# Performance work log

Hardware: AMD Instinct MI355X
Metric: run time of the kernel (lower is better)

Reference implementation:

```python
import jax, jax.numpy as jnp
import numpy as np

EMBED_DIM = 1024
NUM_HEADS = 16
HEAD_DIM = EMBED_DIM // NUM_HEADS


def setup_inputs() -> dict:
    key = jax.random.key(0)
    ks = jax.random.split(key, 11)
    L, N, E = 2048, 4, EMBED_DIM
    s = 1.0 / np.sqrt(E)
    return {
        "query": jax.random.normal(ks[0], (L, N, E), jnp.float32),
        "key": jax.random.normal(ks[1], (L, N, E), jnp.float32),
        "value": jax.random.normal(ks[2], (L, N, E), jnp.float32),
        "Wq": jax.random.normal(ks[3], (E, E), jnp.float32) * s,
        "bq": jax.random.normal(ks[4], (E,), jnp.float32) * s,
        "Wk": jax.random.normal(ks[5], (E, E), jnp.float32) * s,
        "bk": jax.random.normal(ks[6], (E,), jnp.float32) * s,
        "Wv": jax.random.normal(ks[7], (E, E), jnp.float32) * s,
        "bv": jax.random.normal(ks[8], (E,), jnp.float32) * s,
        "Wo": jax.random.normal(ks[9], (E, E), jnp.float32) * s,
        "bo": jax.random.normal(ks[10], (E,), jnp.float32) * s,
    }


def reference(query, key, value, Wq, bq, Wk, bk, Wv, bv, Wo, bo):
    # query/key/value: [L, N, E] (seq-first, as in nn.MultiheadAttention)
    L, N, E = query.shape
    H, D = NUM_HEADS, HEAD_DIM
    scaling = float(D) ** -0.5

    # nn.Linear: x @ W.T + b
    q = (query @ Wq.T + bq) * scaling           # [L, N, E]
    k = key @ Wk.T + bk                          # [S, N, E]
    v = value @ Wv.T + bv                        # [S, N, E]

    S = k.shape[0]
    # [L, N, E] -> [N*H, L, D]
    q = q.reshape(L, N * H, D).transpose(1, 0, 2)
    k = k.reshape(S, N * H, D).transpose(1, 0, 2)
    v = v.reshape(S, N * H, D).transpose(1, 0, 2)

    # attention scores: [N*H, L, S]
    scores = jnp.einsum('bld,bsd->bls', q, k)
    attn = jax.nn.softmax(scores, axis=-1)       # dropout p=0.0 (eval)

    out = jnp.einsum('bls,bsd->bld', attn, v)    # [N*H, L, D]
    out = out.transpose(1, 0, 2).reshape(L, N, E)
    attn_output = out @ Wo.T + bo                # [L, N, E]

    # need_weights=True: average attention over heads -> [N, L, S]
    avg_weights = attn.reshape(N, H, L, S).sum(axis=1) / H
    return attn_output, avg_weights
```

## Files before the change

### kernel.cpp

```cpp
#include <hip/hip_runtime.h>
#include <stdint.h>


typedef __attribute__((ext_vector_type(8))) short bf16x8;
typedef __attribute__((ext_vector_type(4))) short s16x4;
typedef __attribute__((ext_vector_type(4))) float f32x4;

#define MFMA(a, b, c) __builtin_amdgcn_mfma_f32_16x16x32_bf16((a), (b), (c), 0, 0, 0)

__device__ __forceinline__ ushort f2bf(float f) {
    uint32_t u = __builtin_bit_cast(uint32_t, f);
    u += 0x7fffu + ((u >> 16) & 1u);
    return (ushort)(u >> 16);
}

__global__ __launch_bounds__(256) void k_prep(
    const float* __restrict__ xq, const float* __restrict__ xk, const float* __restrict__ xv,
    const float* __restrict__ wq, const float* __restrict__ wk,
    const float* __restrict__ wv, const float* __restrict__ wo,
    ushort* __restrict__ xqb, ushort* __restrict__ xkb, ushort* __restrict__ xvb,
    ushort* __restrict__ wqb, ushort* __restrict__ wkb,
    ushort* __restrict__ wvb, ushort* __restrict__ wob)
{
    const int z = blockIdx.y;
    const float* src; ushort* dst; int n8;
    switch (z) {
        case 0: src = xq; dst = xqb; n8 = 1048576; break;
        case 1: src = xk; dst = xkb; n8 = 1048576; break;
        case 2: src = xv; dst = xvb; n8 = 1048576; break;
        case 3: src = wq; dst = wqb; n8 = 131072;  break;
        case 4: src = wk; dst = wkb; n8 = 131072;  break;
        case 5: src = wv; dst = wvb; n8 = 131072;  break;
        default: src = wo; dst = wob; n8 = 131072; break;
    }
    int u = blockIdx.x * 256 + threadIdx.x;
    if (u >= n8) return;
    const float4* s4 = (const float4*)src;
    float4 a = s4[2 * (size_t)u];
    float4 b = s4[2 * (size_t)u + 1];
    uint4 o;
    o.x = (uint)f2bf(a.x) | ((uint)f2bf(a.y) << 16);
    o.y = (uint)f2bf(a.z) | ((uint)f2bf(a.w) << 16);
    o.z = (uint)f2bf(b.x) | ((uint)f2bf(b.y) << 16);
    o.w = (uint)f2bf(b.z) | ((uint)f2bf(b.w) << 16);
    *(uint4*)(dst + 8 * (size_t)u) = o;
}

__global__ __launch_bounds__(256) void k_proj(
    const ushort* __restrict__ Xq, const ushort* __restrict__ Xk, const ushort* __restrict__ Xv,
    const ushort* __restrict__ Wqb, const ushort* __restrict__ Wkb, const ushort* __restrict__ Wvb,
    const float* __restrict__ bq, const float* __restrict__ bk, const float* __restrict__ bv,
    ushort* __restrict__ Qa, ushort* __restrict__ Ka, ushort* __restrict__ Vt)
{
    const int z = blockIdx.z;
    const ushort* X = (z == 0) ? Xq : (z == 1) ? Xk : Xv;
    const ushort* W = (z == 0) ? Wqb : (z == 1) ? Wkb : Wvb;
    const float* B = (z == 0) ? bq : (z == 1) ? bk : bv;

    __shared__ __align__(16) ushort xt[128][40];
    __shared__ __align__(16) ushort wt[128][40];

    const int t = threadIdx.x;
    const int lane = t & 63;
    const int w = t >> 6;
    const int wr = w >> 1, wc = w & 1;
    const int c = lane & 15, g = lane >> 4;

    const int xrow0 = blockIdx.x * 128;
    const int wrow0 = blockIdx.y * 128;

    f32x4 acc[4][4] = {};

    for (int kt = 0; kt < 32; ++kt) {
        const int k0 = kt * 32;
        __syncthreads();
#pragma unroll
        for (int i = 0; i < 2; ++i) {
            int slot = t + i * 256;
            int row = slot >> 2, seg = slot & 3;
            *(uint4*)&xt[row][seg * 8] =
                *(const uint4*)(X + (size_t)(xrow0 + row) * 1024 + k0 + seg * 8);
            *(uint4*)&wt[row][seg * 8] =
                *(const uint4*)(W + (size_t)(wrow0 + row) * 1024 + k0 + seg * 8);
        }
        __syncthreads();

        const ushort (*At)[40] = (z == 2) ? wt : xt;
        const ushort (*Bt)[40] = (z == 2) ? xt : wt;
        bf16x8 af[4], bfr[4];
#pragma unroll
        for (int m = 0; m < 4; ++m) af[m]  = *(const bf16x8*)&At[wr * 64 + m * 16 + c][g * 8];
#pragma unroll
        for (int n = 0; n < 4; ++n) bfr[n] = *(const bf16x8*)&Bt[wc * 64 + n * 16 + c][g * 8];
#pragma unroll
        for (int m = 0; m < 4; ++m)
#pragma unroll
            for (int n = 0; n < 4; ++n)
                acc[m][n] = MFMA(af[m], bfr[n], acc[m][n]);
    }

    const float QS = 0.125f * 1.44269504088896340736f;
#pragma unroll
    for (int m = 0; m < 4; ++m)
#pragma unroll
        for (int n = 0; n < 4; ++n)
#pragma unroll
            for (int i = 0; i < 4; ++i) {
                int rowi = ((z == 2) ? wrow0 : xrow0) + wr * 64 + m * 16 + 4 * g + i;
                int coli = ((z == 2) ? xrow0 : wrow0) + wc * 64 + n * 16 + c;
                int e = (z == 2) ? rowi : coli;
                int r = (z == 2) ? coli : rowi;
                float v = acc[m][n][i] + B[e];
                if (z == 0) v *= QS;
                ushort bv16 = f2bf(v);
                int nn = r & 3, l = r >> 2, h = e >> 6, d = e & 63;
                int bh = nn * 16 + h;
                if (z == 2) Vt[((size_t)bh * 64 + d) * 2048 + l] = bv16;
                else {
                    ushort* o = (z == 0) ? Qa : Ka;
                    o[((size_t)bh * 2048 + l) * 64 + d] = bv16;
                }
            }
}

__global__ __launch_bounds__(512) void k_attn(
    const ushort* __restrict__ Qa, const ushort* __restrict__ Ka, const ushort* __restrict__ Vt,
    ushort* __restrict__ ctx, float* __restrict__ mbuf, float* __restrict__ lbuf)
{
    __shared__ __align__(16) ushort smem[4608 * 2 + 8 * 16 * 72];
    ushort (*kt)[72] = (ushort(*)[72])smem;
    ushort (*vt)[72] = (ushort(*)[72])(smem + 4608);

    const int t = threadIdx.x;
    const int lane = t & 63;
    const int w = t >> 6;
    const int c = lane & 15, g = lane >> 4;
    ushort* ptw = smem + 9216 + w * 1152;
    const int bh = blockIdx.y;
    const int n = bh >> 4, h = bh & 15;
    const int l0 = blockIdx.x * 128;
    const int lrow = l0 + w * 16 + c;

    bf16x8 aq0 = *(const bf16x8*)(Qa + ((size_t)bh * 2048 + lrow) * 64 + g * 8);
    bf16x8 aq1 = *(const bf16x8*)(Qa + ((size_t)bh * 2048 + lrow) * 64 + 32 + g * 8);

    f32x4 O[4] = {};
    float m = -1e30f, l = 0.f;

    for (int st = 0; st < 32; ++st) {
        __syncthreads();
        {
            int row = t >> 3, seg = t & 7;
            *(uint4*)&kt[row][seg * 8] =
                *(const uint4*)(Ka + ((size_t)bh * 2048 + st * 64 + row) * 64 + seg * 8);
            *(uint4*)&vt[row][seg * 8] =
                *(const uint4*)(Vt + ((size_t)bh * 64 + row) * 2048 + st * 64 + seg * 8);
        }
        __syncthreads();

        f32x4 sc[4];
#pragma unroll
        for (int ct = 0; ct < 4; ++ct) {
            bf16x8 kb0 = *(const bf16x8*)&kt[ct * 16 + c][g * 8];
            bf16x8 kb1 = *(const bf16x8*)&kt[ct * 16 + c][32 + g * 8];
            f32x4 z = {};
            z = MFMA(kb0, aq0, z);
            sc[ct] = MFMA(kb1, aq1, z);
        }

        float pm = fmaxf(fmaxf(sc[0][0], sc[0][1]), fmaxf(sc[0][2], sc[0][3]));
#pragma unroll
        for (int ct = 1; ct < 4; ++ct)
            pm = fmaxf(pm, fmaxf(fmaxf(sc[ct][0], sc[ct][1]), fmaxf(sc[ct][2], sc[ct][3])));
        pm = fmaxf(pm, __shfl_xor(pm, 16));
        pm = fmaxf(pm, __shfl_xor(pm, 32));

        float mn = fmaxf(m, pm);
        float al = exp2f(m - mn);
        m = mn;
        l *= al;
        O[0] *= al; O[1] *= al; O[2] *= al; O[3] *= al;

#pragma unroll
        for (int ct = 0; ct < 4; ++ct) {
            float p0 = exp2f(sc[ct][0] - m);
            float p1 = exp2f(sc[ct][1] - m);
            float p2 = exp2f(sc[ct][2] - m);
            float p3 = exp2f(sc[ct][3] - m);
            l += (p0 + p1) + (p2 + p3);
            uint pa, pb;
            asm("v_cvt_pk_bf16_f32 %0, %1, %2" : "=v"(pa) : "v"(p0), "v"(p1));
            asm("v_cvt_pk_bf16_f32 %0, %1, %2" : "=v"(pb) : "v"(p2), "v"(p3));
            uint64_t pk = (uint64_t)pa | ((uint64_t)pb << 32);
            *(s16x4*)&ptw[c * 72 + ct * 16 + g * 4] = __builtin_bit_cast(s16x4, pk);
        }

        bf16x8 ap0 = *(const bf16x8*)&ptw[c * 72 + g * 8];
        bf16x8 ap1 = *(const bf16x8*)&ptw[c * 72 + 32 + g * 8];
#pragma unroll
        for (int dt = 0; dt < 4; ++dt) {
            bf16x8 vb0 = *(const bf16x8*)&vt[dt * 16 + c][g * 8];
            bf16x8 vb1 = *(const bf16x8*)&vt[dt * 16 + c][32 + g * 8];
            O[dt] = MFMA(vb0, ap0, O[dt]);
            O[dt] = MFMA(vb1, ap1, O[dt]);
        }
    }

    float lsum = l;
    lsum += __shfl_xor(lsum, 16);
    lsum += __shfl_xor(lsum, 32);
    float rl = 1.0f / lsum;

    __syncthreads();
    float* otw = (float*)smem + w * 1040;
#pragma unroll
    for (int dt = 0; dt < 4; ++dt)
#pragma unroll
        for (int r = 0; r < 4; ++r)
            otw[c * 65 + dt * 16 + 4 * g + r] = O[dt][r] * rl;
#pragma unroll
    for (int qq = 0; qq < 16; ++qq) {
        float v = otw[qq * 65 + lane];
        int lr2 = l0 + w * 16 + qq;
        ctx[((size_t)lr2 * 4 + n) * 1024 + h * 64 + lane] = f2bf(v);
    }
    if (g == 0) {
        mbuf[(size_t)bh * 2048 + l0 + w * 16 + c] = m;
        lbuf[(size_t)bh * 2048 + l0 + w * 16 + c] = lsum;
    }
}

__global__ __launch_bounds__(256) void k_oproj(
    const ushort* __restrict__ ctx, const ushort* __restrict__ Wob,
    const float* __restrict__ bo, float* __restrict__ out)
{
    __shared__ __align__(16) ushort xt[128][40];
    __shared__ __align__(16) ushort wt[128][40];

    const int t = threadIdx.x;
    const int lane = t & 63;
    const int w = t >> 6;
    const int wr = w >> 1, wc = w & 1;
    const int c = lane & 15, g = lane >> 4;

    const int r0 = blockIdx.x * 128;
    const int e0 = blockIdx.y * 128;

    f32x4 acc[4][4] = {};

    for (int kt = 0; kt < 32; ++kt) {
        const int k0 = kt * 32;
        __syncthreads();
#pragma unroll
        for (int i = 0; i < 2; ++i) {
            int slot = t + i * 256;
            int row = slot >> 2, seg = slot & 3;
            *(uint4*)&xt[row][seg * 8] =
                *(const uint4*)(ctx + (size_t)(r0 + row) * 1024 + k0 + seg * 8);
            *(uint4*)&wt[row][seg * 8] =
                *(const uint4*)(Wob + (size_t)(e0 + row) * 1024 + k0 + seg * 8);
        }
        __syncthreads();

        bf16x8 af[4], bfr[4];
#pragma unroll
        for (int m = 0; m < 4; ++m) af[m]  = *(const bf16x8*)&xt[wr * 64 + m * 16 + c][g * 8];
#pragma unroll
        for (int n = 0; n < 4; ++n) bfr[n] = *(const bf16x8*)&wt[wc * 64 + n * 16 + c][g * 8];
#pragma unroll
        for (int m = 0; m < 4; ++m)
#pragma unroll
            for (int n = 0; n < 4; ++n)
                acc[m][n] = MFMA(af[m], bfr[n], acc[m][n]);
    }

#pragma unroll
    for (int m = 0; m < 4; ++m)
#pragma unroll
        for (int n = 0; n < 4; ++n)
#pragma unroll
            for (int i = 0; i < 4; ++i) {
                int r = r0 + wr * 64 + m * 16 + 4 * g + i;
                int e = e0 + wc * 64 + n * 16 + c;
                out[(size_t)r * 1024 + e] = acc[m][n][i] + bo[e];
            }
}

__global__ __launch_bounds__(512) void k_avg(
    const ushort* __restrict__ Qa, const ushort* __restrict__ Ka,
    const float* __restrict__ mbuf, const float* __restrict__ lbuf,
    float* __restrict__ avg)
{
    __shared__ float ms[16][64];
    __shared__ float rs[16][64];

    const int t = threadIdx.x;
    const int lane = t & 63;
    const int w = t >> 6;
    const int wr = w >> 2, wc = w & 3;
    const int c = lane & 15, g = lane >> 4;
    const int n = blockIdx.z;
    const int l0 = blockIdx.y * 64;
    const int s0 = blockIdx.x * 512 + wc * 128;

    for (int idx = t; idx < 1024; idx += 512) {
        int hh = idx >> 6, row = idx & 63;
        ms[hh][row] = mbuf[(size_t)(n * 16 + hh) * 2048 + l0 + row];
        rs[hh][row] = 1.0f / (16.0f * lbuf[(size_t)(n * 16 + hh) * 2048 + l0 + row]);
    }
    __syncthreads();

    f32x4 acc[2][8] = {};

    for (int h = 0; h < 16; ++h) {
        const int bh = n * 16 + h;
        bf16x8 aq[2][2];
#pragma unroll
        for (int rt = 0; rt < 2; ++rt) {
            int row = l0 + wr * 32 + rt * 16 + c;
            aq[rt][0] = *(const bf16x8*)(Qa + ((size_t)bh * 2048 + row) * 64 + g * 8);
            aq[rt][1] = *(const bf16x8*)(Qa + ((size_t)bh * 2048 + row) * 64 + 32 + g * 8);
        }
        float mr[8], rl[8];
#pragma unroll
        for (int rt = 0; rt < 2; ++rt)
#pragma unroll
            for (int i = 0; i < 4; ++i) {
                mr[rt * 4 + i] = ms[h][wr * 32 + rt * 16 + 4 * g + i];
                rl[rt * 4 + i] = rs[h][wr * 32 + rt * 16 + 4 * g + i];
            }
#pragma unroll
        for (int ct = 0; ct < 8; ++ct) {
            int srow = s0 + ct * 16 + c;
            bf16x8 b0 = *(const bf16x8*)(Ka + ((size_t)bh * 2048 + srow) * 64 + g * 8);
            bf16x8 b1 = *(const bf16x8*)(Ka + ((size_t)bh * 2048 + srow) * 64 + 32 + g * 8);
#pragma unroll
            for (int rt = 0; rt < 2; ++rt) {
                f32x4 zf = {};
                zf = MFMA(aq[rt][0], b0, zf);
                zf = MFMA(aq[rt][1], b1, zf);
#pragma unroll
                for (int i = 0; i < 4; ++i)
                    acc[rt][ct][i] += exp2f(zf[i] - mr[rt * 4 + i]) * rl[rt * 4 + i];
            }
        }
    }

#pragma unroll
    for (int rt = 0; rt < 2; ++rt)
#pragma unroll
        for (int i = 0; i < 4; ++i) {
            int row = l0 + wr * 32 + rt * 16 + 4 * g + i;
#pragma unroll
            for (int ct = 0; ct < 8; ++ct)
                avg[((size_t)n * 2048 + row) * 2048 + s0 + ct * 16 + c] = acc[rt][ct][i];
        }
}

extern "C" void kernel_launch(void* const* d_in, const int* in_sizes, int n_in,
                              void* d_out, int out_size, void* d_ws, size_t ws_size,
                              hipStream_t stream)
{
    const float* query = (const float*)d_in[0];
    const float* key   = (const float*)d_in[1];
    const float* value = (const float*)d_in[2];
    const float* Wq = (const float*)d_in[3];
    const float* bq = (const float*)d_in[4];
    const float* Wk = (const float*)d_in[5];
    const float* bk = (const float*)d_in[6];
    const float* Wv = (const float*)d_in[7];
    const float* bv = (const float*)d_in[8];
    const float* Wo = (const float*)d_in[9];
    const float* bo = (const float*)d_in[10];

    float* out = (float*)d_out;
    float* avg = out + 8388608;

    ushort* Qa = (ushort*)d_ws;
    ushort* Ka = Qa + 8388608;
    float* mbuf = (float*)(Ka + 8388608);
    float* lbuf = mbuf + 131072;

    ushort* ob  = (ushort*)out;
    ushort* av16 = (ushort*)avg;
    ushort* Xbq = ob;
    ushort* Xbk = ob + 8388608;
    ushort* Vt  = av16;
    ushort* Xbv = av16 + 8388608;
    ushort* Wqb = av16 + 16777216;
    ushort* Wkb = Wqb + 1048576;
    ushort* Wvb = Wkb + 1048576;
    ushort* Wob = Wvb + 1048576;
    ushort* ctx = av16 + 25165824;

    k_prep<<<dim3(4096, 7), 256, 0, stream>>>(query, key, value, Wq, Wk, Wv, Wo,
                                              Xbq, Xbk, Xbv, Wqb, Wkb, Wvb, Wob);
    k_proj<<<dim3(64, 8, 3), 256, 0, stream>>>(Xbq, Xbk, Xbv, Wqb, Wkb, Wvb,
                                               bq, bk, bv, Qa, Ka, Vt);
    k_attn<<<dim3(16, 64), 512, 0, stream>>>(Qa, Ka, Vt, ctx, mbuf, lbuf);
    k_oproj<<<dim3(64, 8), 256, 0, stream>>>(ctx, Wob, bo, out);
    k_avg<<<dim3(4, 32, 4), 512, 0, stream>>>(Qa, Ka, mbuf, lbuf, avg);
}
```

Measured before the change: 620.9 us.

## Retile head-averaged attention kernel into smaller tiles and fold normalizer into exponent

Each warp in the head-averaged attention-weights kernel now computes one 16x64 tile instead of 32x128, and the grid grows fourfold so there are more, lighter blocks. The per-row 1/(16*l) factor is folded into the max term as a log2 offset, so each element needs only exp2 of a difference with no extra multiply. Occupancy is raised via launch bounds and fewer accumulator registers. The cost is more redundant loading of Q and K across blocks and a log2 per row.

Measured after the change: 732.5 us. +18.0%, slower.

```diff
diff --git a/kernel.cpp b/kernel.cpp
--- a/kernel.cpp
+++ b/kernel.cpp
@@ -286,74 +286,59 @@
             }
 }
 
-__global__ __launch_bounds__(512) void k_avg(
+__global__ __launch_bounds__(512, 8) void k_avg(
     const ushort* __restrict__ Qa, const ushort* __restrict__ Ka,
     const float* __restrict__ mbuf, const float* __restrict__ lbuf,
     float* __restrict__ avg)
 {
-    __shared__ float ms[16][64];
-    __shared__ float rs[16][64];
+    __shared__ float ms2[16][64];
 
     const int t = threadIdx.x;
     const int lane = t & 63;
     const int w = t >> 6;
-    const int wr = w >> 2, wc = w & 3;
+    const int wr = w & 3, wc = w >> 2;
     const int c = lane & 15, g = lane >> 4;
     const int n = blockIdx.z;
     const int l0 = blockIdx.y * 64;
-    const int s0 = blockIdx.x * 512 + wc * 128;
+    const int s0 = blockIdx.x * 128;
 
     for (int idx = t; idx < 1024; idx += 512) {
         int hh = idx >> 6, row = idx & 63;
-        ms[hh][row] = mbuf[(size_t)(n * 16 + hh) * 2048 + l0 + row];
-        rs[hh][row] = 1.0f / (16.0f * lbuf[(size_t)(n * 16 + hh) * 2048 + l0 + row]);
+        float mv = mbuf[(size_t)(n * 16 + hh) * 2048 + l0 + row];
+        float lv = lbuf[(size_t)(n * 16 + hh) * 2048 + l0 + row];
+        ms2[hh][row] = mv + __log2f(16.0f * lv);
     }
     __syncthreads();
 
-    f32x4 acc[2][8] = {};
+    f32x4 acc[4] = {};
+    const ushort* qp = Qa + ((size_t)(n * 16) * 2048 + l0 + wr * 16 + c) * 64 + g * 8;
+    const ushort* kp0 = Ka + ((size_t)(n * 16) * 2048 + s0 + wc * 64 + c) * 64 + g * 8;
 
     for (int h = 0; h < 16; ++h) {
-        const int bh = n * 16 + h;
-        bf16x8 aq[2][2];
-#pragma unroll
-        for (int rt = 0; rt < 2; ++rt) {
-            int row = l0 + wr * 32 + rt * 16 + c;
-            aq[rt][0] = *(const bf16x8*)(Qa + ((size_t)bh * 2048 + row) * 64 + g * 8);
-            aq[rt][1] = *(const bf16x8*)(Qa + ((size_t)bh * 2048 + row) * 64 + 32 + g * 8);
-        }
-        float mr[8], rl[8];
-#pragma unroll
-        for (int rt = 0; rt < 2; ++rt)
-#pragma unroll
-            for (int i = 0; i < 4; ++i) {
-                mr[rt * 4 + i] = ms[h][wr * 32 + rt * 16 + 4 * g + i];
-                rl[rt * 4 + i] = rs[h][wr * 32 + rt * 16 + 4 * g + i];
-            }
-#pragma unroll
-        for (int ct = 0; ct < 8; ++ct) {
-            int srow = s0 + ct * 16 + c;
-            bf16x8 b0 = *(const bf16x8*)(Ka + ((size_t)bh * 2048 + srow) * 64 + g * 8);
-            bf16x8 b1 = *(const bf16x8*)(Ka + ((size_t)bh * 2048 + srow) * 64 + 32 + g * 8);
-#pragma unroll
-            for (int rt = 0; rt < 2; ++rt) {
-                f32x4 zf = {};
-                zf = MFMA(aq[rt][0], b0, zf);
-                zf = MFMA(aq[rt][1], b1, zf);
-#pragma unroll
-                for (int i = 0; i < 4; ++i)
-                    acc[rt][ct][i] += exp2f(zf[i] - mr[rt * 4 + i]) * rl[rt * 4 + i];
-            }
-        }
-    }
-
-#pragma unroll
-    for (int rt = 0; rt < 2; ++rt)
+        const size_t hoff = (size_t)h * 2048 * 64;
+        bf16x8 aq0 = *(const bf16x8*)(qp + hoff);
+        bf16x8 aq1 = *(const bf16x8*)(qp + hoff + 32);
+        f32x4 mr2 = *(const f32x4*)&ms2[h][wr * 16 + 4 * g];
+#pragma unroll
+        for (int ct = 0; ct < 4; ++ct) {
+            const ushort* kp = kp0 + hoff + (size_t)ct * 16 * 64;
+            bf16x8 b0 = *(const bf16x8*)kp;
+            bf16x8 b1 = *(const bf16x8*)(kp + 32);
+            f32x4 zf = {};
+            zf = MFMA(aq0, b0, zf);
+            zf = MFMA(aq1, b1, zf);
+#pragma unroll
+            for (int i = 0; i < 4; ++i)
+                acc[ct][i] += exp2f(zf[i] - mr2[i]);
+        }
+    }
+
+#pragma unroll
+    for (int ct = 0; ct < 4; ++ct)
 #pragma unroll
         for (int i = 0; i < 4; ++i) {
-            int row = l0 + wr * 32 + rt * 16 + 4 * g + i;
-#pragma unroll
-            for (int ct = 0; ct < 8; ++ct)
-                avg[((size_t)n * 2048 + row) * 2048 + s0 + ct * 16 + c] = acc[rt][ct][i];
+            int row = l0 + wr * 16 + 4 * g + i;
+            avg[((size_t)n * 2048 + row) * 2048 + s0 + wc * 64 + ct * 16 + c] = acc[ct][i];
         }
 }
 
@@ -399,5 +384,5 @@
                                                bq, bk, bv, Qa, Ka, Vt);
     k_attn<<<dim3(16, 64), 512, 0, stream>>>(Qa, Ka, Vt, ctx, mbuf, lbuf);
     k_oproj<<<dim3(64, 8), 256, 0, stream>>>(ctx, Wob, bo, out);
-    k_avg<<<dim3(4, 32, 4), 512, 0, stream>>>(Qa, Ka, mbuf, lbuf, avg);
-}
+    k_avg<<<dim3(16, 32, 4), 512, 0, stream>>>(Qa, Ka, mbuf, lbuf, avg);
+}
```
